# Performance work log

Hardware: AMD Instinct MI355X
Metric: run time of the kernel (lower is better)

## Reference

```python
import jax, jax.numpy as jnp
import numpy as np

N = 50000   # nodes
E = 800000  # edges per layer
D = 128     # feature dim
H = 256     # mlp hidden
O = 3       # output dim


def setup_inputs() -> dict:
    key = jax.random.key(0)
    ks = jax.random.split(key, 16)
    def lin(k, fan_out, fan_in):
        s = 1.0 / np.sqrt(fan_in)
        kw, kb = jax.random.split(k)
        return (jax.random.uniform(kw, (fan_out, fan_in), jnp.float32, -s, s),
                jax.random.uniform(kb, (fan_out,), jnp.float32, -s, s))
    x = jax.random.normal(ks[0], (N, D), jnp.float32)
    edge_idx0 = jax.random.randint(ks[1], (2, E), 0, N, dtype=jnp.int64)
    edge_idx1 = jax.random.randint(ks[2], (2, E), 0, N, dtype=jnp.int64)
    Wl1, bl1 = lin(ks[3], D, D)   # SAGE layer1: lin_l (aggregated neighbors, with bias)
    Wr1, _ = lin(ks[4], D, D)     # SAGE layer1: lin_r (root, no bias)
    Wl2, bl2 = lin(ks[5], D, D)
    Wr2, _ = lin(ks[6], D, D)
    Ws, bs = lin(ks[7], D, D)     # skip_fc
    W1, b1 = lin(ks[8], H, D)     # mlp hidden
    W2, b2 = lin(ks[9], O, H)     # mlp out
    return dict(x=x, edge_idx0=edge_idx0, edge_idx1=edge_idx1,
                Wl1=Wl1, bl1=bl1, Wr1=Wr1, Wl2=Wl2, bl2=bl2, Wr2=Wr2,
                Ws=Ws, bs=bs, W1=W1, b1=b1, W2=W2, b2=b2)


def _sage(x, ei, Wl, bl, Wr):
    # PyG SAGEConv with mean aggregation: out = lin_l(mean_j x_j) + lin_r(x_i)
    src, dst = ei[0], ei[1]
    agg = jax.ops.segment_sum(x[src], dst, num_segments=N)          # [N, D] gather-scatter
    cnt = jax.ops.segment_sum(jnp.ones((ei.shape[1],), x.dtype), dst, num_segments=N)
    agg = agg / jnp.maximum(cnt, 1.0)[:, None]
    return agg @ Wl.T + bl + x @ Wr.T


def reference(x, edge_idx0, edge_idx1, Wl1, bl1, Wr1, Wl2, bl2, Wr2,
              Ws, bs, W1, b1, W2, b2):
    inp = x
    h = _sage(x, edge_idx0, Wl1, bl1, Wr1)
    h = _sage(h, edge_idx1, Wl2, bl2, Wr2)
    h = h + (inp @ Ws.T + bs)            # skip connection
    h = jax.nn.relu(h @ W1.T + b1)       # MLP head
    return h @ W2.T + b2                  # [N, 3]
```

## Files before the change

kernel.cpp:

```cpp
#include <hip/hip_runtime.h>
#include <hip/hip_bf16.h>


#define DD 128
#define SB 8
#define CH 4096
typedef unsigned short u16;
typedef __attribute__((ext_vector_type(8))) short short8;
typedef __attribute__((ext_vector_type(4))) float f32x4;

__device__ inline u16 f2bf(float f) {
    __hip_bfloat16 h = __float2bfloat16(f);
    u16 u;
    __builtin_memcpy(&u, &h, 2);
    return u;
}
__device__ inline unsigned pack2(float lo, float hi) {
    return (unsigned)f2bf(lo) | ((unsigned)f2bf(hi) << 16);
}
__device__ inline float bf_lo(unsigned u) { union { unsigned x; float f; } c; c.x = u << 16; return c.f; }
__device__ inline float bf_hi(unsigned u) { union { unsigned x; float f; } c; c.x = u & 0xffff0000u; return c.f; }

struct CastJobs {
    const float4* src[6];
    uint2* dst[6];
    int qstart[7];
};

__global__ __launch_bounds__(256) void hist1_kernel(CastJobs jb,
                                                    const int* __restrict__ dst0, int* __restrict__ h0,
                                                    const int* __restrict__ dst1, int* __restrict__ h1,
                                                    int e0, int e1, int nb, int P) {
    int bx = blockIdx.x;
    int t = threadIdx.x;
    if (bx >= P) {
        if (blockIdx.y == 0) {
            int q = (bx - P) * 256 + t;
            if (q < jb.qstart[6]) {
                int i = 0;
#pragma unroll
                for (int k = 1; k < 6; ++k) if (q >= jb.qstart[k]) i = k;
                int local = q - jb.qstart[i];
                float4 v = jb.src[i][local];
                jb.dst[i][local] = make_uint2(pack2(v.x, v.y), pack2(v.z, v.w));
            }
        }
        return;
    }
    int arr = blockIdx.y;
    const int* dst = arr ? dst1 : dst0;
    int* hist = arr ? h1 : h0;
    int e = arr ? e1 : e0;
    __shared__ int h[256];
    h[t] = 0;
    __syncthreads();
    int base = bx * CH;
    int hi = min(base + CH, e);
    for (int i = base + t; i < hi; i += 256) atomicAdd(&h[dst[i] >> SB], 1);
    __syncthreads();
    if (t < nb) hist[t * P + bx] = h[t];
}

__global__ __launch_bounds__(256) void scan_kernel(int* __restrict__ h0, int* __restrict__ bs0,
                                                   int* __restrict__ h1, int* __restrict__ bs1,
                                                   int P) {
    int arr = blockIdx.y;
    int* hist = arr ? h1 : h0;
    int* bs = arr ? bs1 : bs0;
    int b = blockIdx.x;
    __shared__ int s[256];
    int t = threadIdx.x;
    int v = (t < P) ? hist[b * P + t] : 0;
    s[t] = v;
    __syncthreads();
    for (int off = 1; off < 256; off <<= 1) {
        int u = (t >= off) ? s[t - off] : 0;
        __syncthreads();
        s[t] += u;
        __syncthreads();
    }
    if (t < P) hist[b * P + t] = s[t] - v;
    if (t == 0) bs[b] = s[255];
}

__global__ __launch_bounds__(256) void scatter1_kernel(
    const int* __restrict__ src0, const int* __restrict__ dst0, const int* __restrict__ h0,
    const int* __restrict__ bs0, unsigned* __restrict__ binned0,
    const int* __restrict__ src1, const int* __restrict__ dst1, const int* __restrict__ h1,
    const int* __restrict__ bs1, unsigned* __restrict__ binned1,
    int e0, int e1, int nb, int P) {
    int arr = blockIdx.y;
    const int* src = arr ? src1 : src0;
    const int* dst = arr ? dst1 : dst0;
    const int* hist = arr ? h1 : h0;
    const int* bs = arr ? bs1 : bs0;
    unsigned* binned = arr ? binned1 : binned0;
    int e = arr ? e1 : e0;
    int p = blockIdx.x;
    __shared__ int cnt[256];
    __shared__ int s[256];
    int t = threadIdx.x;
    int v = (t < nb) ? bs[t] : 0;
    s[t] = v;
    __syncthreads();
    for (int off = 1; off < 256; off <<= 1) {
        int u = (t >= off) ? s[t - off] : 0;
        __syncthreads();
        s[t] += u;
        __syncthreads();
    }
    if (t < nb) cnt[t] = hist[t * P + p] + (s[t] - v);
    __syncthreads();
    int base = p * CH;
    int hi = min(base + CH, e);
    for (int i = base + t; i < hi; i += 256) {
        int d = dst[i];
        int pos = atomicAdd(&cnt[d >> SB], 1);
        binned[pos] = ((unsigned)d << 16) | (unsigned)src[i];
    }
}

__global__ __launch_bounds__(256) void place_kernel(
    const unsigned* __restrict__ binned0, const int* __restrict__ bs0, int* __restrict__ rp0, u16* __restrict__ csr0,
    const unsigned* __restrict__ binned1, const int* __restrict__ bs1, int* __restrict__ rp1, u16* __restrict__ csr1,
    int e0, int e1, int n, int nb) {
    int arr = blockIdx.y;
    const unsigned* binned = arr ? binned1 : binned0;
    const int* bs = arr ? bs1 : bs0;
    int* rp = arr ? rp1 : rp0;
    u16* csr = arr ? csr1 : csr0;
    int E = arr ? e1 : e0;
    int b = blockIdx.x;
    __shared__ int cnt[256];
    __shared__ int s[256];
    int t = threadIdx.x;
    s[t] = (t < nb) ? bs[t] : 0;
    __syncthreads();
    for (int off = 1; off < 256; off <<= 1) {
        int u = (t >= off) ? s[t - off] : 0;
        __syncthreads();
        s[t] += u;
        __syncthreads();
    }
    int base = (b > 0) ? s[b - 1] : 0;
    int end = s[b];
    if (b == nb - 1 && t == 0) rp[n] = E;
    __syncthreads();
    cnt[t] = 0;
    __syncthreads();
    for (int i = base + t; i < end; i += 256)
        atomicAdd(&cnt[(binned[i] >> 16) & 255], 1);
    __syncthreads();
    int deg = cnt[t];
    s[t] = deg;
    __syncthreads();
    for (int off = 1; off < 256; off <<= 1) {
        int u = (t >= off) ? s[t - off] : 0;
        __syncthreads();
        s[t] += u;
        __syncthreads();
    }
    int gpos = base + s[t] - deg;
    int node = (b << SB) + t;
    if (node < n) rp[node] = gpos;
    cnt[t] = gpos;
    __syncthreads();
    for (int i = base + t; i < end; i += 256) {
        unsigned pk = binned[i];
        int ld = (pk >> 16) & 255;
        int pos = atomicAdd(&cnt[ld], 1);
        csr[pos] = (u16)(pk & 0xffffu);
    }
}

__global__ __launch_bounds__(256) void agg1_kernel(const u16* __restrict__ G1,
                                                   const u16* __restrict__ csr,
                                                   const int* __restrict__ rp,
                                                   const float* __restrict__ bl1,
                                                   u16* __restrict__ h1, int n) {
    int g = (blockIdx.x * 256 + threadIdx.x) >> 5;
    int lane = threadIdx.x & 31;
    if (g >= n) return;
    int start = rp[g], end = rp[g + 1];
    int d = end - start;
    const uint2* X2 = (const uint2*)G1;
    float a0 = 0.f, a1 = 0.f, a2 = 0.f, a3 = 0.f;
    int e = start;
    for (; e + 3 < end; e += 4) {
        int s0 = csr[e], s1 = csr[e + 1], s2 = csr[e + 2], s3 = csr[e + 3];
        uint2 v0 = X2[(size_t)s0 * 96 + lane];
        uint2 v1 = X2[(size_t)s1 * 96 + lane];
        uint2 v2 = X2[(size_t)s2 * 96 + lane];
        uint2 v3 = X2[(size_t)s3 * 96 + lane];
        a0 += (bf_lo(v0.x) + bf_lo(v1.x)) + (bf_lo(v2.x) + bf_lo(v3.x));
        a1 += (bf_hi(v0.x) + bf_hi(v1.x)) + (bf_hi(v2.x) + bf_hi(v3.x));
        a2 += (bf_lo(v0.y) + bf_lo(v1.y)) + (bf_lo(v2.y) + bf_lo(v3.y));
        a3 += (bf_hi(v0.y) + bf_hi(v1.y)) + (bf_hi(v2.y) + bf_hi(v3.y));
    }
    for (; e < end; ++e) {
        uint2 v0 = X2[(size_t)csr[e] * 96 + lane];
        a0 += bf_lo(v0.x); a1 += bf_hi(v0.x);
        a2 += bf_lo(v0.y); a3 += bf_hi(v0.y);
    }
    float sc = 1.0f / (float)max(d, 1);
    uint2 m = X2[(size_t)g * 96 + 32 + lane];
    float4 b = ((const float4*)bl1)[lane];
    uint2 r;
    r.x = pack2(a0 * sc + bf_lo(m.x) + b.x, a1 * sc + bf_hi(m.x) + b.y);
    r.y = pack2(a2 * sc + bf_lo(m.y) + b.z, a3 * sc + bf_hi(m.y) + b.w);
    ((uint2*)h1)[(size_t)g * 32 + lane] = r;
}

__global__ __launch_bounds__(256) void agg2_kernel(const u16* __restrict__ G2,
                                                   const u16* __restrict__ G1,
                                                   const u16* __restrict__ csr,
                                                   const int* __restrict__ rp,
                                                   const float* __restrict__ bl2,
                                                   const float* __restrict__ bs,
                                                   u16* __restrict__ h3, int n) {
    int g = (blockIdx.x * 256 + threadIdx.x) >> 5;
    int lane = threadIdx.x & 31;
    if (g >= n) return;
    int start = rp[g], end = rp[g + 1];
    int d = end - start;
    const uint2* X2 = (const uint2*)G2;
    float a0 = 0.f, a1 = 0.f, a2 = 0.f, a3 = 0.f;
    int e = start;
    for (; e + 3 < end; e += 4) {
        int s0 = csr[e], s1 = csr[e + 1], s2 = csr[e + 2], s3 = csr[e + 3];
        uint2 v0 = X2[(size_t)s0 * 64 + lane];
        uint2 v1 = X2[(size_t)s1 * 64 + lane];
        uint2 v2 = X2[(size_t)s2 * 64 + lane];
        uint2 v3 = X2[(size_t)s3 * 64 + lane];
        a0 += (bf_lo(v0.x) + bf_lo(v1.x)) + (bf_lo(v2.x) + bf_lo(v3.x));
        a1 += (bf_hi(v0.x) + bf_hi(v1.x)) + (bf_hi(v2.x) + bf_hi(v3.x));
        a2 += (bf_lo(v0.y) + bf_lo(v1.y)) + (bf_lo(v2.y) + bf_lo(v3.y));
        a3 += (bf_hi(v0.y) + bf_hi(v1.y)) + (bf_hi(v2.y) + bf_hi(v3.y));
    }
    for (; e < end; ++e) {
        uint2 v0 = X2[(size_t)csr[e] * 64 + lane];
        a0 += bf_lo(v0.x); a1 += bf_hi(v0.x);
        a2 += bf_lo(v0.y); a3 += bf_hi(v0.y);
    }
    float sc = 1.0f / (float)max(d, 1);
    uint2 m2 = X2[(size_t)g * 64 + 32 + lane];
    uint2 m1 = ((const uint2*)G1)[(size_t)g * 96 + 64 + lane];
    float4 cb = ((const float4*)bl2)[lane];
    float4 sb = ((const float4*)bs)[lane];
    uint2 r;
    r.x = pack2(a0 * sc + bf_lo(m2.x) + bf_lo(m1.x) + cb.x + sb.x,
                a1 * sc + bf_hi(m2.x) + bf_hi(m1.x) + cb.y + sb.y);
    r.y = pack2(a2 * sc + bf_lo(m2.y) + bf_lo(m1.y) + cb.z + sb.z,
                a3 * sc + bf_hi(m2.y) + bf_hi(m1.y) + cb.w + sb.w);
    ((uint2*)h3)[(size_t)g * 32 + lane] = r;
}

template <bool F32A>
__global__ __launch_bounds__(256) void mfma_gemm(const void* __restrict__ Av,
                                                 const u16* __restrict__ W,
                                                 u16* __restrict__ C, int M, int NC) {
    __shared__ u16 Bs[32 * 512];
    const int t = threadIdx.x;
    const int colBase = blockIdx.y * 128;
#pragma unroll
    for (int i = 0; i < 8; ++i) {
        int id = t + 256 * i;
        int nrow = id >> 4, cc = id & 15;
        int f = ((nrow >> 4) << 2) | (cc >> 2);
        int dl = ((cc & 3) << 4) | (nrow & 15);
        *(uint4*)&Bs[(f * 64 + dl) * 8] = ((const uint4*)W)[(size_t)(colBase + nrow) * 16 + cc];
    }
    __syncthreads();
    const int w = t >> 6, lane = t & 63, r = lane & 15, half = lane >> 4;
    short8 bf[32];
#pragma unroll
    for (int f = 0; f < 32; ++f)
        bf[f] = *(const short8*)&Bs[(f * 64 + lane) * 8];
    const int nTiles = M >> 4;
    const int nWaves = gridDim.x * 4;
    for (int tile = blockIdx.x * 4 + w; tile < nTiles; tile += nWaves) {
        int rowA = (tile << 4) + r;
        short8 af[4];
        if (F32A) {
            const float4* Arow = (const float4*)Av + (size_t)rowA * 32 + half * 2;
#pragma unroll
            for (int kk = 0; kk < 4; ++kk) {
                float4 a = Arow[kk * 8], b = Arow[kk * 8 + 1];
                uint4 v = make_uint4(pack2(a.x, a.y), pack2(a.z, a.w),
                                     pack2(b.x, b.y), pack2(b.z, b.w));
                af[kk] = *(short8*)&v;
            }
        } else {
            const uint4* Arow = (const uint4*)Av + (size_t)rowA * 16 + half;
#pragma unroll
            for (int kk = 0; kk < 4; ++kk) {
                uint4 v = Arow[kk * 4];
                af[kk] = *(short8*)&v;
            }
        }
        f32x4 acc[8];
#pragma unroll
        for (int i = 0; i < 8; ++i) acc[i] = (f32x4){0.f, 0.f, 0.f, 0.f};
#pragma unroll
        for (int kk = 0; kk < 4; ++kk)
#pragma unroll
            for (int ct = 0; ct < 8; ++ct)
                acc[ct] = __builtin_amdgcn_mfma_f32_16x16x32_bf16(af[kk], bf[ct * 4 + kk], acc[ct], 0, 0, 0);
#pragma unroll
        for (int ct = 0; ct < 8; ++ct) {
            int col = colBase + ct * 16 + r;
#pragma unroll
            for (int reg = 0; reg < 4; ++reg) {
                int row = (tile << 4) + half * 4 + reg;
                C[(size_t)row * NC + col] = f2bf(acc[ct][reg]);
            }
        }
    }
}

__global__ __launch_bounds__(256) void gemm_out_kernel(const u16* __restrict__ h3,
                                                       const u16* __restrict__ W1,
                                                       const float* __restrict__ b1,
                                                       const float* __restrict__ W2,
                                                       const float* __restrict__ b2,
                                                       float* __restrict__ out, int M) {
    __shared__ u16 Bs[64 * 512];
    __shared__ float w2s[3 * 256];
    __shared__ float b1s[256];
    const int t = threadIdx.x;
#pragma unroll
    for (int i = 0; i < 16; ++i) {
        int id = t + 256 * i;
        int nrow = id >> 4, cc = id & 15;
        int f = ((nrow >> 4) << 2) | (cc >> 2);
        int dl = ((cc & 3) << 4) | (nrow & 15);
        *(uint4*)&Bs[(f * 64 + dl) * 8] = ((const uint4*)W1)[(size_t)nrow * 16 + cc];
    }
    for (int i = t; i < 768; i += 256) w2s[i] = W2[i];
    b1s[t] = b1[t];
    __syncthreads();
    const int w = t >> 6, lane = t & 63, r = lane & 15, half = lane >> 4;
    const int nTiles = M >> 4;
    const int nWaves = gridDim.x * 4;
    const u16* bB = &Bs[lane * 8];
    float c0 = b2[0], c1 = b2[1], c2 = b2[2];
    for (int tile = blockIdx.x * 4 + w; tile < nTiles; tile += nWaves) {
        int rowA = (tile << 4) + r;
        const uint4* Arow = (const uint4*)h3 + (size_t)rowA * 16 + half;
        short8 af[4];
#pragma unroll
        for (int kk = 0; kk < 4; ++kk) {
            uint4 v = Arow[kk * 4];
            af[kk] = *(short8*)&v;
        }
        f32x4 acc[16];
#pragma unroll
        for (int i = 0; i < 16; ++i) acc[i] = (f32x4){0.f, 0.f, 0.f, 0.f};
#pragma unroll
        for (int kk = 0; kk < 4; ++kk)
#pragma unroll
            for (int ct = 0; ct < 16; ++ct) {
                short8 bf = *(const short8*)(bB + (ct * 4 + kk) * 512);
                acc[ct] = __builtin_amdgcn_mfma_f32_16x16x32_bf16(af[kk], bf, acc[ct], 0, 0, 0);
            }
        float p[4][3] = {{0.f, 0.f, 0.f}, {0.f, 0.f, 0.f}, {0.f, 0.f, 0.f}, {0.f, 0.f, 0.f}};
#pragma unroll
        for (int ct = 0; ct < 16; ++ct) {
            int col = ct * 16 + r;
            float bv = b1s[col];
            float w0 = w2s[col], w1 = w2s[256 + col], w2v = w2s[512 + col];
#pragma unroll
            for (int reg = 0; reg < 4; ++reg) {
                float h4 = fmaxf(acc[ct][reg] + bv, 0.f);
                p[reg][0] += h4 * w0;
                p[reg][1] += h4 * w1;
                p[reg][2] += h4 * w2v;
            }
        }
#pragma unroll
        for (int m = 1; m < 16; m <<= 1)
#pragma unroll
            for (int reg = 0; reg < 4; ++reg) {
                p[reg][0] += __shfl_xor(p[reg][0], m);
                p[reg][1] += __shfl_xor(p[reg][1], m);
                p[reg][2] += __shfl_xor(p[reg][2], m);
            }
        if (r == 0) {
#pragma unroll
            for (int reg = 0; reg < 4; ++reg) {
                int row = (tile << 4) + half * 4 + reg;
                out[(size_t)row * 3 + 0] = p[reg][0] + c0;
                out[(size_t)row * 3 + 1] = p[reg][1] + c1;
                out[(size_t)row * 3 + 2] = p[reg][2] + c2;
            }
        }
    }
}

extern "C" void kernel_launch(void* const* d_in, const int* in_sizes, int n_in,
                              void* d_out, int out_size, void* d_ws, size_t ws_size,
                              hipStream_t stream) {
    const float* x   = (const float*)d_in[0];
    const int*   ei0 = (const int*)d_in[1];
    const int*   ei1 = (const int*)d_in[2];
    const float* Wl1 = (const float*)d_in[3];
    const float* bl1 = (const float*)d_in[4];
    const float* Wr1 = (const float*)d_in[5];
    const float* Wl2 = (const float*)d_in[6];
    const float* bl2 = (const float*)d_in[7];
    const float* Wr2 = (const float*)d_in[8];
    const float* Wsk = (const float*)d_in[9];
    const float* bsk = (const float*)d_in[10];
    const float* W1  = (const float*)d_in[11];
    const float* b1  = (const float*)d_in[12];
    const float* W2  = (const float*)d_in[13];
    const float* b2  = (const float*)d_in[14];
    float* out = (float*)d_out;

    const int N  = in_sizes[0] / DD;
    const int E0 = in_sizes[1] / 2;
    const int E1 = in_sizes[2] / 2;
    const int H  = in_sizes[12];

    const int* src0 = ei0;      const int* dst0 = ei0 + E0;
    const int* src1 = ei1;      const int* dst1 = ei1 + E1;

    const int nb   = (N + 255) >> SB;
    const int Emax = (E0 > E1) ? E0 : E1;
    const int P    = (Emax + CH - 1) / CH;

    char* wp = (char*)d_ws;
    auto carve = [&](size_t bytes) { char* p = wp; wp += (bytes + 255) & ~(size_t)255; return p; };
    u16* G1   = (u16*)carve((size_t)N * 384 * 2);
    u16* G2   = (u16*)carve((size_t)N * 256 * 2);
    u16* h1h  = (u16*)carve((size_t)N * DD * 2);
    u16* h3h  = (u16*)carve((size_t)N * DD * 2);
    u16* wc1  = (u16*)carve((size_t)384 * DD * 2);
    u16* wc2  = (u16*)carve((size_t)256 * DD * 2);
    u16* w1h  = (u16*)carve((size_t)H * DD * 2);
    int* rp0  = (int*)carve((size_t)(N + 1) * 4);
    int* rp1  = (int*)carve((size_t)(N + 1) * 4);
    u16* csr0 = (u16*)carve((size_t)E0 * 2);
    u16* csr1 = (u16*)carve((size_t)E1 * 2);
    unsigned* binned0 = (unsigned*)carve((size_t)E0 * 4);
    unsigned* binned1 = (unsigned*)carve((size_t)E1 * 4);
    int* hist1_0 = (int*)carve((size_t)nb * P * 4);
    int* hist1_1 = (int*)carve((size_t)nb * P * 4);
    int* bsum0 = (int*)carve((size_t)nb * 4);
    int* bsum1 = (int*)carve((size_t)nb * 4);

    CastJobs jb;
    const float* srcs[6] = {Wl1, Wr1, Wsk, Wl2, Wr2, W1};
    u16* dsts[6] = {wc1, wc1 + 128 * DD, wc1 + 256 * DD, wc2, wc2 + 128 * DD, w1h};
    int  cnts[6] = {DD * DD, DD * DD, DD * DD, DD * DD, DD * DD, H * DD};
    int q = 0;
    for (int i = 0; i < 6; ++i) {
        jb.src[i] = (const float4*)srcs[i];
        jb.dst[i] = (uint2*)dsts[i];
        jb.qstart[i] = q;
        q += cnts[i] / 4;
    }
    jb.qstart[6] = q;
    const int CB = (q + 255) / 256;

    const int gAgg = (N * 32 + 255) / 256;

    hist1_kernel<<<dim3(P + CB, 2), 256, 0, stream>>>(jb, dst0, hist1_0, dst1, hist1_1, E0, E1, nb, P);
    scan_kernel<<<dim3(nb, 2), 256, 0, stream>>>(hist1_0, bsum0, hist1_1, bsum1, P);
    scatter1_kernel<<<dim3(P, 2), 256, 0, stream>>>(src0, dst0, hist1_0, bsum0, binned0,
                                                    src1, dst1, hist1_1, bsum1, binned1, E0, E1, nb, P);
    place_kernel<<<dim3(nb, 2), 256, 0, stream>>>(binned0, bsum0, rp0, csr0,
                                                  binned1, bsum1, rp1, csr1, E0, E1, N, nb);

    mfma_gemm<true><<<dim3(320, 3), 256, 0, stream>>>(x, wc1, G1, N, 384);
    agg1_kernel<<<gAgg, 256, 0, stream>>>(G1, csr0, rp0, bl1, h1h, N);
    mfma_gemm<false><<<dim3(320, 2), 256, 0, stream>>>(h1h, wc2, G2, N, 256);
    agg2_kernel<<<gAgg, 256, 0, stream>>>(G2, G1, csr1, rp1, bl2, bsk, h3h, N);
    gemm_out_kernel<<<512, 256, 0, stream>>>(h3h, w1h, b1, W2, b2, out, N);
}
```

Measured before the change: 256.2 us.

## Fuse CSR build, GEMMs and aggregations into one cooperative persistent kernel

Replaces the nine separate launches (histogram, scan, scatter, place, two GEMMs, two aggregations) with a single cooperative mega-kernel that uses grid.sync between phases. Blocks are split so that some build the CSR structure while the others convert weights and run the first x-projection GEMM in parallel, which overlaps independent work and removes launch gaps. The GEMMs now read B fragments from LDS per MFMA instead of holding them all in registers, to allow 4 blocks per CU. The cost is grid-wide barriers and possibly slower inner GEMM loops due to repeated LDS reads.

```diff
diff --git a/kernel.cpp b/kernel.cpp
--- a/kernel.cpp
+++ b/kernel.cpp
@@ -1,5 +1,8 @@
 #include <hip/hip_runtime.h>
 #include <hip/hip_bf16.h>
+#include <hip/hip_cooperative_groups.h>
+
+namespace cg = cooperative_groups;
 
 
 #define DD 128
@@ -27,276 +30,37 @@
     int qstart[7];
 };
 
-__global__ __launch_bounds__(256) void hist1_kernel(CastJobs jb,
-                                                    const int* __restrict__ dst0, int* __restrict__ h0,
-                                                    const int* __restrict__ dst1, int* __restrict__ h1,
-                                                    int e0, int e1, int nb, int P) {
-    int bx = blockIdx.x;
-    int t = threadIdx.x;
-    if (bx >= P) {
-        if (blockIdx.y == 0) {
-            int q = (bx - P) * 256 + t;
-            if (q < jb.qstart[6]) {
-                int i = 0;
-#pragma unroll
-                for (int k = 1; k < 6; ++k) if (q >= jb.qstart[k]) i = k;
-                int local = q - jb.qstart[i];
-                float4 v = jb.src[i][local];
-                jb.dst[i][local] = make_uint2(pack2(v.x, v.y), pack2(v.z, v.w));
-            }
-        }
-        return;
-    }
-    int arr = blockIdx.y;
-    const int* dst = arr ? dst1 : dst0;
-    int* hist = arr ? h1 : h0;
-    int e = arr ? e1 : e0;
-    __shared__ int h[256];
-    h[t] = 0;
-    __syncthreads();
-    int base = bx * CH;
-    int hi = min(base + CH, e);
-    for (int i = base + t; i < hi; i += 256) atomicAdd(&h[dst[i] >> SB], 1);
-    __syncthreads();
-    if (t < nb) hist[t * P + bx] = h[t];
-}
-
-__global__ __launch_bounds__(256) void scan_kernel(int* __restrict__ h0, int* __restrict__ bs0,
-                                                   int* __restrict__ h1, int* __restrict__ bs1,
-                                                   int P) {
-    int arr = blockIdx.y;
-    int* hist = arr ? h1 : h0;
-    int* bs = arr ? bs1 : bs0;
-    int b = blockIdx.x;
-    __shared__ int s[256];
-    int t = threadIdx.x;
-    int v = (t < P) ? hist[b * P + t] : 0;
-    s[t] = v;
-    __syncthreads();
-    for (int off = 1; off < 256; off <<= 1) {
-        int u = (t >= off) ? s[t - off] : 0;
-        __syncthreads();
-        s[t] += u;
-        __syncthreads();
-    }
-    if (t < P) hist[b * P + t] = s[t] - v;
-    if (t == 0) bs[b] = s[255];
-}
-
-__global__ __launch_bounds__(256) void scatter1_kernel(
-    const int* __restrict__ src0, const int* __restrict__ dst0, const int* __restrict__ h0,
-    const int* __restrict__ bs0, unsigned* __restrict__ binned0,
-    const int* __restrict__ src1, const int* __restrict__ dst1, const int* __restrict__ h1,
-    const int* __restrict__ bs1, unsigned* __restrict__ binned1,
-    int e0, int e1, int nb, int P) {
-    int arr = blockIdx.y;
-    const int* src = arr ? src1 : src0;
-    const int* dst = arr ? dst1 : dst0;
-    const int* hist = arr ? h1 : h0;
-    const int* bs = arr ? bs1 : bs0;
-    unsigned* binned = arr ? binned1 : binned0;
-    int e = arr ? e1 : e0;
-    int p = blockIdx.x;
-    __shared__ int cnt[256];
-    __shared__ int s[256];
-    int t = threadIdx.x;
-    int v = (t < nb) ? bs[t] : 0;
-    s[t] = v;
-    __syncthreads();
-    for (int off = 1; off < 256; off <<= 1) {
-        int u = (t >= off) ? s[t - off] : 0;
-        __syncthreads();
-        s[t] += u;
-        __syncthreads();
-    }
-    if (t < nb) cnt[t] = hist[t * P + p] + (s[t] - v);
-    __syncthreads();
-    int base = p * CH;
-    int hi = min(base + CH, e);
-    for (int i = base + t; i < hi; i += 256) {
-        int d = dst[i];
-        int pos = atomicAdd(&cnt[d >> SB], 1);
-        binned[pos] = ((unsigned)d << 16) | (unsigned)src[i];
-    }
-}
-
-__global__ __launch_bounds__(256) void place_kernel(
-    const unsigned* __restrict__ binned0, const int* __restrict__ bs0, int* __restrict__ rp0, u16* __restrict__ csr0,
-    const unsigned* __restrict__ binned1, const int* __restrict__ bs1, int* __restrict__ rp1, u16* __restrict__ csr1,
-    int e0, int e1, int n, int nb) {
-    int arr = blockIdx.y;
-    const unsigned* binned = arr ? binned1 : binned0;
-    const int* bs = arr ? bs1 : bs0;
-    int* rp = arr ? rp1 : rp0;
-    u16* csr = arr ? csr1 : csr0;
-    int E = arr ? e1 : e0;
-    int b = blockIdx.x;
-    __shared__ int cnt[256];
-    __shared__ int s[256];
-    int t = threadIdx.x;
-    s[t] = (t < nb) ? bs[t] : 0;
-    __syncthreads();
-    for (int off = 1; off < 256; off <<= 1) {
-        int u = (t >= off) ? s[t - off] : 0;
-        __syncthreads();
-        s[t] += u;
-        __syncthreads();
-    }
-    int base = (b > 0) ? s[b - 1] : 0;
-    int end = s[b];
-    if (b == nb - 1 && t == 0) rp[n] = E;
-    __syncthreads();
-    cnt[t] = 0;
-    __syncthreads();
-    for (int i = base + t; i < end; i += 256)
-        atomicAdd(&cnt[(binned[i] >> 16) & 255], 1);
-    __syncthreads();
-    int deg = cnt[t];
-    s[t] = deg;
-    __syncthreads();
-    for (int off = 1; off < 256; off <<= 1) {
-        int u = (t >= off) ? s[t - off] : 0;
-        __syncthreads();
-        s[t] += u;
-        __syncthreads();
-    }
-    int gpos = base + s[t] - deg;
-    int node = (b << SB) + t;
-    if (node < n) rp[node] = gpos;
-    cnt[t] = gpos;
-    __syncthreads();
-    for (int i = base + t; i < end; i += 256) {
-        unsigned pk = binned[i];
-        int ld = (pk >> 16) & 255;
-        int pos = atomicAdd(&cnt[ld], 1);
-        csr[pos] = (u16)(pk & 0xffffu);
-    }
-}
-
-__global__ __launch_bounds__(256) void agg1_kernel(const u16* __restrict__ G1,
-                                                   const u16* __restrict__ csr,
-                                                   const int* __restrict__ rp,
-                                                   const float* __restrict__ bl1,
-                                                   u16* __restrict__ h1, int n) {
-    int g = (blockIdx.x * 256 + threadIdx.x) >> 5;
-    int lane = threadIdx.x & 31;
-    if (g >= n) return;
-    int start = rp[g], end = rp[g + 1];
-    int d = end - start;
-    const uint2* X2 = (const uint2*)G1;
-    float a0 = 0.f, a1 = 0.f, a2 = 0.f, a3 = 0.f;
-    int e = start;
-    for (; e + 3 < end; e += 4) {
-        int s0 = csr[e], s1 = csr[e + 1], s2 = csr[e + 2], s3 = csr[e + 3];
-        uint2 v0 = X2[(size_t)s0 * 96 + lane];
-        uint2 v1 = X2[(size_t)s1 * 96 + lane];
-        uint2 v2 = X2[(size_t)s2 * 96 + lane];
-        uint2 v3 = X2[(size_t)s3 * 96 + lane];
-        a0 += (bf_lo(v0.x) + bf_lo(v1.x)) + (bf_lo(v2.x) + bf_lo(v3.x));
-        a1 += (bf_hi(v0.x) + bf_hi(v1.x)) + (bf_hi(v2.x) + bf_hi(v3.x));
-        a2 += (bf_lo(v0.y) + bf_lo(v1.y)) + (bf_lo(v2.y) + bf_lo(v3.y));
-        a3 += (bf_hi(v0.y) + bf_hi(v1.y)) + (bf_hi(v2.y) + bf_hi(v3.y));
-    }
-    for (; e < end; ++e) {
-        uint2 v0 = X2[(size_t)csr[e] * 96 + lane];
-        a0 += bf_lo(v0.x); a1 += bf_hi(v0.x);
-        a2 += bf_lo(v0.y); a3 += bf_hi(v0.y);
-    }
-    float sc = 1.0f / (float)max(d, 1);
-    uint2 m = X2[(size_t)g * 96 + 32 + lane];
-    float4 b = ((const float4*)bl1)[lane];
-    uint2 r;
-    r.x = pack2(a0 * sc + bf_lo(m.x) + b.x, a1 * sc + bf_hi(m.x) + b.y);
-    r.y = pack2(a2 * sc + bf_lo(m.y) + b.z, a3 * sc + bf_hi(m.y) + b.w);
-    ((uint2*)h1)[(size_t)g * 32 + lane] = r;
-}
-
-__global__ __launch_bounds__(256) void agg2_kernel(const u16* __restrict__ G2,
-                                                   const u16* __restrict__ G1,
-                                                   const u16* __restrict__ csr,
-                                                   const int* __restrict__ rp,
-                                                   const float* __restrict__ bl2,
-                                                   const float* __restrict__ bs,
-                                                   u16* __restrict__ h3, int n) {
-    int g = (blockIdx.x * 256 + threadIdx.x) >> 5;
-    int lane = threadIdx.x & 31;
-    if (g >= n) return;
-    int start = rp[g], end = rp[g + 1];
-    int d = end - start;
-    const uint2* X2 = (const uint2*)G2;
-    float a0 = 0.f, a1 = 0.f, a2 = 0.f, a3 = 0.f;
-    int e = start;
-    for (; e + 3 < end; e += 4) {
-        int s0 = csr[e], s1 = csr[e + 1], s2 = csr[e + 2], s3 = csr[e + 3];
-        uint2 v0 = X2[(size_t)s0 * 64 + lane];
-        uint2 v1 = X2[(size_t)s1 * 64 + lane];
-        uint2 v2 = X2[(size_t)s2 * 64 + lane];
-        uint2 v3 = X2[(size_t)s3 * 64 + lane];
-        a0 += (bf_lo(v0.x) + bf_lo(v1.x)) + (bf_lo(v2.x) + bf_lo(v3.x));
-        a1 += (bf_hi(v0.x) + bf_hi(v1.x)) + (bf_hi(v2.x) + bf_hi(v3.x));
-        a2 += (bf_lo(v0.y) + bf_lo(v1.y)) + (bf_lo(v2.y) + bf_lo(v3.y));
-        a3 += (bf_hi(v0.y) + bf_hi(v1.y)) + (bf_hi(v2.y) + bf_hi(v3.y));
-    }
-    for (; e < end; ++e) {
-        uint2 v0 = X2[(size_t)csr[e] * 64 + lane];
-        a0 += bf_lo(v0.x); a1 += bf_hi(v0.x);
-        a2 += bf_lo(v0.y); a3 += bf_hi(v0.y);
-    }
-    float sc = 1.0f / (float)max(d, 1);
-    uint2 m2 = X2[(size_t)g * 64 + 32 + lane];
-    uint2 m1 = ((const uint2*)G1)[(size_t)g * 96 + 64 + lane];
-    float4 cb = ((const float4*)bl2)[lane];
-    float4 sb = ((const float4*)bs)[lane];
-    uint2 r;
-    r.x = pack2(a0 * sc + bf_lo(m2.x) + bf_lo(m1.x) + cb.x + sb.x,
-                a1 * sc + bf_hi(m2.x) + bf_hi(m1.x) + cb.y + sb.y);
-    r.y = pack2(a2 * sc + bf_lo(m2.y) + bf_lo(m1.y) + cb.z + sb.z,
-                a3 * sc + bf_hi(m2.y) + bf_hi(m1.y) + cb.w + sb.w);
-    ((uint2*)h3)[(size_t)g * 32 + lane] = r;
-}
-
-template <bool F32A>
-__global__ __launch_bounds__(256) void mfma_gemm(const void* __restrict__ Av,
-                                                 const u16* __restrict__ W,
-                                                 u16* __restrict__ C, int M, int NC) {
-    __shared__ u16 Bs[32 * 512];
-    const int t = threadIdx.x;
-    const int colBase = blockIdx.y * 128;
-#pragma unroll
-    for (int i = 0; i < 8; ++i) {
-        int id = t + 256 * i;
-        int nrow = id >> 4, cc = id & 15;
-        int f = ((nrow >> 4) << 2) | (cc >> 2);
-        int dl = ((cc & 3) << 4) | (nrow & 15);
-        *(uint4*)&Bs[(f * 64 + dl) * 8] = ((const uint4*)W)[(size_t)(colBase + nrow) * 16 + cc];
-    }
-    __syncthreads();
-    const int w = t >> 6, lane = t & 63, r = lane & 15, half = lane >> 4;
-    short8 bf[32];
-#pragma unroll
-    for (int f = 0; f < 32; ++f)
-        bf[f] = *(const short8*)&Bs[(f * 64 + lane) * 8];
-    const int nTiles = M >> 4;
-    const int nWaves = gridDim.x * 4;
-    for (int tile = blockIdx.x * 4 + w; tile < nTiles; tile += nWaves) {
+struct MegaArgs {
+    CastJobs jb;
+    const float* x;
+    const int* src0; const int* dst0;
+    const int* src1; const int* dst1;
+    int* hist0; int* hist1;
+    int* bsum0; int* bsum1;
+    unsigned* binned0; unsigned* binned1;
+    int* rp0; int* rp1;
+    u16* csr0; u16* csr1;
+    const u16* wc1; const u16* wc2;
+    u16* G1; u16* G2; u16* h1h; u16* h3h;
+    const float* bl1; const float* bl2; const float* bsk;
+    int E0, E1, N, nb, P, CSRB;
+};
+
+__device__ __forceinline__ void gemm_f32A(const float* x, const u16* Bs, u16* C,
+                                          int lo, int hi, int wsid, int nws,
+                                          int colBase, int lane, int NC) {
+    int r = lane & 15, half = lane >> 4;
+    const u16* bB = Bs + lane * 8;
+    for (int tile = lo + wsid; tile < hi; tile += nws) {
         int rowA = (tile << 4) + r;
+        const float4* Arow = (const float4*)x + (size_t)rowA * 32 + half * 2;
         short8 af[4];
-        if (F32A) {
-            const float4* Arow = (const float4*)Av + (size_t)rowA * 32 + half * 2;
-#pragma unroll
-            for (int kk = 0; kk < 4; ++kk) {
-                float4 a = Arow[kk * 8], b = Arow[kk * 8 + 1];
-                uint4 v = make_uint4(pack2(a.x, a.y), pack2(a.z, a.w),
-                                     pack2(b.x, b.y), pack2(b.z, b.w));
-                af[kk] = *(short8*)&v;
-            }
-        } else {
-            const uint4* Arow = (const uint4*)Av + (size_t)rowA * 16 + half;
-#pragma unroll
-            for (int kk = 0; kk < 4; ++kk) {
-                uint4 v = Arow[kk * 4];
-                af[kk] = *(short8*)&v;
-            }
+#pragma unroll
+        for (int kk = 0; kk < 4; ++kk) {
+            float4 aa = Arow[kk * 8], bb = Arow[kk * 8 + 1];
+            uint4 v = make_uint4(pack2(aa.x, aa.y), pack2(aa.z, aa.w),
+                                 pack2(bb.x, bb.y), pack2(bb.z, bb.w));
+            af[kk] = *(short8*)&v;
         }
         f32x4 acc[8];
 #pragma unroll
@@ -304,8 +68,10 @@
 #pragma unroll
         for (int kk = 0; kk < 4; ++kk)
 #pragma unroll
-            for (int ct = 0; ct < 8; ++ct)
-                acc[ct] = __builtin_amdgcn_mfma_f32_16x16x32_bf16(af[kk], bf[ct * 4 + kk], acc[ct], 0, 0, 0);
+            for (int ct = 0; ct < 8; ++ct) {
+                short8 bf = *(const short8*)(bB + (ct * 4 + kk) * 512);
+                acc[ct] = __builtin_amdgcn_mfma_f32_16x16x32_bf16(af[kk], bf, acc[ct], 0, 0, 0);
+            }
 #pragma unroll
         for (int ct = 0; ct < 8; ++ct) {
             int col = colBase + ct * 16 + r;
@@ -313,6 +79,308 @@
             for (int reg = 0; reg < 4; ++reg) {
                 int row = (tile << 4) + half * 4 + reg;
                 C[(size_t)row * NC + col] = f2bf(acc[ct][reg]);
+            }
+        }
+    }
+}
+
+__device__ __forceinline__ void gemm_bf16A(const u16* A, const u16* Bs, u16* C,
+                                           int lo, int hi, int wsid, int nws,
+                                           int colBase, int lane, int NC) {
+    int r = lane & 15, half = lane >> 4;
+    const u16* bB = Bs + lane * 8;
+    for (int tile = lo + wsid; tile < hi; tile += nws) {
+        int rowA = (tile << 4) + r;
+        const uint4* Arow = (const uint4*)A + (size_t)rowA * 16 + half;
+        short8 af[4];
+#pragma unroll
+        for (int kk = 0; kk < 4; ++kk) {
+            uint4 v = Arow[kk * 4];
+            af[kk] = *(short8*)&v;
+        }
+        f32x4 acc[8];
+#pragma unroll
+        for (int i = 0; i < 8; ++i) acc[i] = (f32x4){0.f, 0.f, 0.f, 0.f};
+#pragma unroll
+        for (int kk = 0; kk < 4; ++kk)
+#pragma unroll
+            for (int ct = 0; ct < 8; ++ct) {
+                short8 bf = *(const short8*)(bB + (ct * 4 + kk) * 512);
+                acc[ct] = __builtin_amdgcn_mfma_f32_16x16x32_bf16(af[kk], bf, acc[ct], 0, 0, 0);
+            }
+#pragma unroll
+        for (int ct = 0; ct < 8; ++ct) {
+            int col = colBase + ct * 16 + r;
+#pragma unroll
+            for (int reg = 0; reg < 4; ++reg) {
+                int row = (tile << 4) + half * 4 + reg;
+                C[(size_t)row * NC + col] = f2bf(acc[ct][reg]);
+            }
+        }
+    }
+}
+
+__global__ __launch_bounds__(256, 4) void mega_kernel(MegaArgs a) {
+    cg::grid_group grid = cg::this_grid();
+    __shared__ u16 Bs[32 * 512];
+    __shared__ int Lc[256];
+    __shared__ int Ls[256];
+    const int t = threadIdx.x;
+    const int b = blockIdx.x;
+    const int G = gridDim.x;
+    const int CSRB = a.CSRB;
+    const bool isCSR = (b < CSRB);
+    const int w = t >> 6, lane = t & 63;
+
+    if (isCSR) {
+        for (int job = b; job < 2 * a.P; job += CSRB) {
+            int arr = job / a.P, p = job % a.P;
+            const int* dst = arr ? a.dst1 : a.dst0;
+            int* hist = arr ? a.hist1 : a.hist0;
+            int e = arr ? a.E1 : a.E0;
+            Lc[t] = 0;
+            __syncthreads();
+            int base = p * CH, hi = min(base + CH, e);
+            for (int i = base + t; i < hi; i += 256) atomicAdd(&Lc[dst[i] >> SB], 1);
+            __syncthreads();
+            if (t < a.nb) hist[t * a.P + p] = Lc[t];
+            __syncthreads();
+        }
+    } else {
+        int nC = G - CSRB;
+        for (int q = (b - CSRB) * 256 + t; q < a.jb.qstart[6]; q += nC * 256) {
+            int i = 0;
+#pragma unroll
+            for (int k = 1; k < 6; ++k) if (q >= a.jb.qstart[k]) i = k;
+            int local = q - a.jb.qstart[i];
+            float4 v = a.jb.src[i][local];
+            a.jb.dst[i][local] = make_uint2(pack2(v.x, v.y), pack2(v.z, v.w));
+        }
+    }
+    grid.sync();
+
+    const int nT1 = a.N >> 4;
+    const int nGB = G - CSRB;
+    const int gj = b - CSRB;
+    const int col1 = isCSR ? 0 : (gj % 3);
+    const int cntc = (nGB + 2 - col1) / 3;
+    const int wsid1 = isCSR ? 0 : ((gj / 3) * 4 + w);
+    const int nws1 = cntc * 4;
+    const int c0 = 0, c1 = nT1 / 3, c2 = (2 * nT1) / 3, c3 = nT1;
+
+    if (isCSR) {
+        for (int job = b; job < 2 * a.nb; job += CSRB) {
+            int arr = job / a.nb, bb = job % a.nb;
+            int* hist = arr ? a.hist1 : a.hist0;
+            int* bsA = arr ? a.bsum1 : a.bsum0;
+            int v = (t < a.P) ? hist[bb * a.P + t] : 0;
+            Ls[t] = v;
+            __syncthreads();
+            for (int off = 1; off < 256; off <<= 1) {
+                int u = (t >= off) ? Ls[t - off] : 0;
+                __syncthreads();
+                Ls[t] += u;
+                __syncthreads();
+            }
+            if (t < a.P) hist[bb * a.P + t] = Ls[t] - v;
+            if (t == 0) bsA[bb] = Ls[255];
+            __syncthreads();
+        }
+    } else {
+#pragma unroll
+        for (int i = 0; i < 8; ++i) {
+            int id = t + 256 * i;
+            int nrow = id >> 4, cc = id & 15;
+            int f = ((nrow >> 4) << 2) | (cc >> 2);
+            int dl = ((cc & 3) << 4) | (nrow & 15);
+            *(uint4*)&Bs[(f * 64 + dl) * 8] = ((const uint4*)a.wc1)[(size_t)(col1 * 128 + nrow) * 16 + cc];
+        }
+        __syncthreads();
+        gemm_f32A(a.x, Bs, a.G1, c0, c1, wsid1, nws1, col1 * 128, lane, 384);
+    }
+    grid.sync();
+
+    if (isCSR) {
+        for (int job = b; job < 2 * a.P; job += CSRB) {
+            int arr = job / a.P, p = job % a.P;
+            const int* src = arr ? a.src1 : a.src0;
+            const int* dst = arr ? a.dst1 : a.dst0;
+            const int* hist = arr ? a.hist1 : a.hist0;
+            const int* bsA = arr ? a.bsum1 : a.bsum0;
+            unsigned* binned = arr ? a.binned1 : a.binned0;
+            int e = arr ? a.E1 : a.E0;
+            int v = (t < a.nb) ? bsA[t] : 0;
+            Ls[t] = v;
+            __syncthreads();
+            for (int off = 1; off < 256; off <<= 1) {
+                int u = (t >= off) ? Ls[t - off] : 0;
+                __syncthreads();
+                Ls[t] += u;
+                __syncthreads();
+            }
+            if (t < a.nb) Lc[t] = hist[t * a.P + p] + (Ls[t] - v);
+            __syncthreads();
+            int base = p * CH, hi = min(base + CH, e);
+            for (int i = base + t; i < hi; i += 256) {
+                int d = dst[i];
+                int pos = atomicAdd(&Lc[d >> SB], 1);
+                binned[pos] = ((unsigned)d << 16) | (unsigned)src[i];
+            }
+            __syncthreads();
+        }
+    } else {
+        gemm_f32A(a.x, Bs, a.G1, c1, c2, wsid1, nws1, col1 * 128, lane, 384);
+    }
+    grid.sync();
+
+    if (isCSR) {
+        for (int job = b; job < 2 * a.nb; job += CSRB) {
+            int arr = job / a.nb, bb = job % a.nb;
+            const unsigned* binned = arr ? a.binned1 : a.binned0;
+            const int* bsA = arr ? a.bsum1 : a.bsum0;
+            int* rp = arr ? a.rp1 : a.rp0;
+            u16* csr = arr ? a.csr1 : a.csr0;
+            int E = arr ? a.E1 : a.E0;
+            Ls[t] = (t < a.nb) ? bsA[t] : 0;
+            __syncthreads();
+            for (int off = 1; off < 256; off <<= 1) {
+                int u = (t >= off) ? Ls[t - off] : 0;
+                __syncthreads();
+                Ls[t] += u;
+                __syncthreads();
+            }
+            int base = (bb > 0) ? Ls[bb - 1] : 0;
+            int end = Ls[bb];
+            if (bb == a.nb - 1 && t == 0) rp[a.N] = E;
+            __syncthreads();
+            Lc[t] = 0;
+            __syncthreads();
+            for (int i = base + t; i < end; i += 256)
+                atomicAdd(&Lc[(binned[i] >> 16) & 255], 1);
+            __syncthreads();
+            int deg = Lc[t];
+            Ls[t] = deg;
+            __syncthreads();
+            for (int off = 1; off < 256; off <<= 1) {
+                int u = (t >= off) ? Ls[t - off] : 0;
+                __syncthreads();
+                Ls[t] += u;
+                __syncthreads();
+            }
+            int gpos = base + Ls[t] - deg;
+            int node = (bb << SB) + t;
+            if (node < a.N) rp[node] = gpos;
+            __syncthreads();
+            Lc[t] = gpos;
+            __syncthreads();
+            for (int i = base + t; i < end; i += 256) {
+                unsigned pk = binned[i];
+                int ld = (pk >> 16) & 255;
+                int pos = atomicAdd(&Lc[ld], 1);
+                csr[pos] = (u16)(pk & 0xffffu);
+            }
+            __syncthreads();
+        }
+    } else {
+        gemm_f32A(a.x, Bs, a.G1, c2, c3, wsid1, nws1, col1 * 128, lane, 384);
+    }
+    grid.sync();
+
+    {
+        int jobs = (a.N + 7) >> 3;
+        int ln = t & 31;
+        for (int job = b; job < jobs; job += G) {
+            int g = (job << 3) + (t >> 5);
+            if (g < a.N) {
+                int start = a.rp0[g], end = a.rp0[g + 1];
+                int d = end - start;
+                const uint2* X2 = (const uint2*)a.G1;
+                float a0 = 0.f, a1 = 0.f, a2 = 0.f, a3 = 0.f;
+                int e = start;
+                for (; e + 3 < end; e += 4) {
+                    int s0 = a.csr0[e], s1 = a.csr0[e + 1], s2 = a.csr0[e + 2], s3 = a.csr0[e + 3];
+                    uint2 v0 = X2[(size_t)s0 * 96 + ln];
+                    uint2 v1 = X2[(size_t)s1 * 96 + ln];
+                    uint2 v2 = X2[(size_t)s2 * 96 + ln];
+                    uint2 v3 = X2[(size_t)s3 * 96 + ln];
+                    a0 += (bf_lo(v0.x) + bf_lo(v1.x)) + (bf_lo(v2.x) + bf_lo(v3.x));
+                    a1 += (bf_hi(v0.x) + bf_hi(v1.x)) + (bf_hi(v2.x) + bf_hi(v3.x));
+                    a2 += (bf_lo(v0.y) + bf_lo(v1.y)) + (bf_lo(v2.y) + bf_lo(v3.y));
+                    a3 += (bf_hi(v0.y) + bf_hi(v1.y)) + (bf_hi(v2.y) + bf_hi(v3.y));
+                }
+                for (; e < end; ++e) {
+                    uint2 v0 = X2[(size_t)a.csr0[e] * 96 + ln];
+                    a0 += bf_lo(v0.x); a1 += bf_hi(v0.x);
+                    a2 += bf_lo(v0.y); a3 += bf_hi(v0.y);
+                }
+                float sc = 1.0f / (float)max(d, 1);
+                uint2 m = X2[(size_t)g * 96 + 32 + ln];
+                float4 bv = ((const float4*)a.bl1)[ln];
+                uint2 r;
+                r.x = pack2(a0 * sc + bf_lo(m.x) + bv.x, a1 * sc + bf_hi(m.x) + bv.y);
+                r.y = pack2(a2 * sc + bf_lo(m.y) + bv.z, a3 * sc + bf_hi(m.y) + bv.w);
+                ((uint2*)a.h1h)[(size_t)g * 32 + ln] = r;
+            }
+        }
+    }
+    grid.sync();
+
+    {
+        int col = b & 1;
+#pragma unroll
+        for (int i = 0; i < 8; ++i) {
+            int id = t + 256 * i;
+            int nrow = id >> 4, cc = id & 15;
+            int f = ((nrow >> 4) << 2) | (cc >> 2);
+            int dl = ((cc & 3) << 4) | (nrow & 15);
+            *(uint4*)&Bs[(f * 64 + dl) * 8] = ((const uint4*)a.wc2)[(size_t)(col * 128 + nrow) * 16 + cc];
+        }
+        __syncthreads();
+        int rg = b >> 1;
+        int wsid = rg * 4 + w;
+        int nws = (G >> 1) * 4;
+        gemm_bf16A(a.h1h, Bs, a.G2, 0, nT1, wsid, nws, col * 128, lane, 256);
+    }
+    grid.sync();
+
+    {
+        int jobs = (a.N + 7) >> 3;
+        int ln = t & 31;
+        for (int job = b; job < jobs; job += G) {
+            int g = (job << 3) + (t >> 5);
+            if (g < a.N) {
+                int start = a.rp1[g], end = a.rp1[g + 1];
+                int d = end - start;
+                const uint2* X2 = (const uint2*)a.G2;
+                float a0 = 0.f, a1 = 0.f, a2 = 0.f, a3 = 0.f;
+                int e = start;
+                for (; e + 3 < end; e += 4) {
+                    int s0 = a.csr1[e], s1 = a.csr1[e + 1], s2 = a.csr1[e + 2], s3 = a.csr1[e + 3];
+                    uint2 v0 = X2[(size_t)s0 * 64 + ln];
+                    uint2 v1 = X2[(size_t)s1 * 64 + ln];
+                    uint2 v2 = X2[(size_t)s2 * 64 + ln];
+                    uint2 v3 = X2[(size_t)s3 * 64 + ln];
+                    a0 += (bf_lo(v0.x) + bf_lo(v1.x)) + (bf_lo(v2.x) + bf_lo(v3.x));
+                    a1 += (bf_hi(v0.x) + bf_hi(v1.x)) + (bf_hi(v2.x) + bf_hi(v3.x));
+                    a2 += (bf_lo(v0.y) + bf_lo(v1.y)) + (bf_lo(v2.y) + bf_lo(v3.y));
+                    a3 += (bf_hi(v0.y) + bf_hi(v1.y)) + (bf_hi(v2.y) + bf_hi(v3.y));
+                }
+                for (; e < end; ++e) {
+                    uint2 v0 = X2[(size_t)a.csr1[e] * 64 + ln];
+                    a0 += bf_lo(v0.x); a1 += bf_hi(v0.x);
+                    a2 += bf_lo(v0.y); a3 += bf_hi(v0.y);
+                }
+                float sc = 1.0f / (float)max(d, 1);
+                uint2 m2 = X2[(size_t)g * 64 + 32 + ln];
+                uint2 m1 = ((const uint2*)a.G1)[(size_t)g * 96 + 64 + ln];
+                float4 cb = ((const float4*)a.bl2)[ln];
+                float4 sb = ((const float4*)a.bsk)[ln];
+                uint2 r;
+                r.x = pack2(a0 * sc + bf_lo(m2.x) + bf_lo(m1.x) + cb.x + sb.x,
+                            a1 * sc + bf_hi(m2.x) + bf_hi(m1.x) + cb.y + sb.y);
+                r.y = pack2(a2 * sc + bf_lo(m2.y) + bf_lo(m1.y) + cb.z + sb.z,
+                            a3 * sc + bf_hi(m2.y) + bf_hi(m1.y) + cb.w + sb.w);
+                ((uint2*)a.h3h)[(size_t)g * 32 + ln] = r;
             }
         }
     }
@@ -449,32 +517,40 @@
     int* bsum0 = (int*)carve((size_t)nb * 4);
     int* bsum1 = (int*)carve((size_t)nb * 4);
 
-    CastJobs jb;
+    MegaArgs ma;
     const float* srcs[6] = {Wl1, Wr1, Wsk, Wl2, Wr2, W1};
     u16* dsts[6] = {wc1, wc1 + 128 * DD, wc1 + 256 * DD, wc2, wc2 + 128 * DD, w1h};
     int  cnts[6] = {DD * DD, DD * DD, DD * DD, DD * DD, DD * DD, H * DD};
     int q = 0;
     for (int i = 0; i < 6; ++i) {
-        jb.src[i] = (const float4*)srcs[i];
-        jb.dst[i] = (uint2*)dsts[i];
-        jb.qstart[i] = q;
+        ma.jb.src[i] = (const float4*)srcs[i];
+        ma.jb.dst[i] = (uint2*)dsts[i];
+        ma.jb.qstart[i] = q;
         q += cnts[i] / 4;
     }
-    jb.qstart[6] = q;
-    const int CB = (q + 255) / 256;
-
-    const int gAgg = (N * 32 + 255) / 256;
-
-    hist1_kernel<<<dim3(P + CB, 2), 256, 0, stream>>>(jb, dst0, hist1_0, dst1, hist1_1, E0, E1, nb, P);
-    scan_kernel<<<dim3(nb, 2), 256, 0, stream>>>(hist1_0, bsum0, hist1_1, bsum1, P);
-    scatter1_kernel<<<dim3(P, 2), 256, 0, stream>>>(src0, dst0, hist1_0, bsum0, binned0,
-                                                    src1, dst1, hist1_1, bsum1, binned1, E0, E1, nb, P);
-    place_kernel<<<dim3(nb, 2), 256, 0, stream>>>(binned0, bsum0, rp0, csr0,
-                                                  binned1, bsum1, rp1, csr1, E0, E1, N, nb);
-
-    mfma_gemm<true><<<dim3(320, 3), 256, 0, stream>>>(x, wc1, G1, N, 384);
-    agg1_kernel<<<gAgg, 256, 0, stream>>>(G1, csr0, rp0, bl1, h1h, N);
-    mfma_gemm<false><<<dim3(320, 2), 256, 0, stream>>>(h1h, wc2, G2, N, 256);
-    agg2_kernel<<<gAgg, 256, 0, stream>>>(G2, G1, csr1, rp1, bl2, bsk, h3h, N);
+    ma.jb.qstart[6] = q;
+
+    ma.x = x;
+    ma.src0 = src0; ma.dst0 = dst0; ma.src1 = src1; ma.dst1 = dst1;
+    ma.hist0 = hist1_0; ma.hist1 = hist1_1;
+    ma.bsum0 = bsum0; ma.bsum1 = bsum1;
+    ma.binned0 = binned0; ma.binned1 = binned1;
+    ma.rp0 = rp0; ma.rp1 = rp1;
+    ma.csr0 = csr0; ma.csr1 = csr1;
+    ma.wc1 = wc1; ma.wc2 = wc2;
+    ma.G1 = G1; ma.G2 = G2; ma.h1h = h1h; ma.h3h = h3h;
+    ma.bl1 = bl1; ma.bl2 = bl2; ma.bsk = bsk;
+    ma.E0 = E0; ma.E1 = E1; ma.N = N; ma.nb = nb; ma.P = P;
+
+    int occ = 0;
+    hipOccupancyMaxActiveBlocksPerMultiprocessor(&occ, mega_kernel, 256, 0);
+    if (occ < 1) occ = 1;
+    int G = occ * 256;
+    if (G > 1024) G = 1024;
+    ma.CSRB = (G >= 784) ? 2 * P : G / 2;
+
+    void* kargs[] = { &ma };
+    hipLaunchCooperativeKernel((void*)mega_kernel, dim3(G), dim3(256), kargs, 0, stream);
+
     gemm_out_kernel<<<512, 256, 0, stream>>>(h3h, w1h, b1, W2, b2, out, N);
 }
```

Measured after the change: 790.0 us. 3.08x slower.
